# Performance work log

Hardware: AMD Instinct MI355X
Metric: run time of the kernel (lower is better)

The kernel has to match this reference:

```python
import jax, jax.numpy as jnp
import numpy as np

NUM_Q = 8
B, N, D = 8, 1024, 512
C = 1024


def setup_inputs() -> dict:
    key = jax.random.key(0)
    k1, k2 = jax.random.split(key)
    x = jax.random.normal(k1, (B, N, D), dtype=jnp.float32)
    codebooks = jax.random.normal(k2, (NUM_Q, C, D), dtype=jnp.float32)
    return {"x": x, "codebooks": codebooks}


def _vq_layer(residual, codebook):
    # residual: [b, n, d]; codebook: [c, d]
    # squared euclidean distances without materializing differences tensor
    r2 = jnp.sum(residual * residual, axis=-1, keepdims=True)          # [b, n, 1]
    e2 = jnp.sum(codebook * codebook, axis=-1)                          # [c]
    dots = jnp.einsum('bnd,cd->bnc', residual, codebook)                # [b, n, c]
    dist = r2 - 2.0 * dots + e2                                         # [b, n, c]
    indices = jnp.argmin(dist, axis=-1)                                 # [b, n] int32
    quantized = codebook[indices]                                       # [b, n, d]
    # straight-through estimator (codebook is EMA-updated, not differentiated)
    quantized_st = residual + jax.lax.stop_gradient(quantized - residual)
    # commitment loss (default commitment_weight = 1.0)
    loss = jnp.mean((jax.lax.stop_gradient(quantized_st) - residual) ** 2)
    return quantized_st, indices, loss


def reference(x, codebooks):
    def step(carry, codebook):
        residual, quantized_out = carry
        quantized, indices, loss = _vq_layer(residual, codebook)
        return (residual - quantized, quantized_out + quantized), (indices, loss)

    init = (x, jnp.zeros_like(x))
    (_, quantized_out), (all_indices, all_losses) = jax.lax.scan(step, init, codebooks)
    # all_indices: [q, b, n] -> [b, n, q]; all_losses: [q]
    all_indices = jnp.transpose(all_indices, (1, 2, 0))
    return quantized_out, all_indices, all_losses
```

## Files before the change

kernel.cpp:

```cpp
#include <hip/hip_runtime.h>
#include <float.h>

#define NUM_Q 8
#define BN    8192
#define D     512
#define C     1024

#define QOUT_OFF 0
#define IDX_OFF  (BN * D)
#define LOSS_OFF (IDX_OFF + BN * NUM_Q)

#define WIN_OFF_B  0
#define E2_OFF_B   (BN * 8)

typedef _Float16 f16x8 __attribute__((ext_vector_type(8)));
typedef float    f32x4 __attribute__((ext_vector_type(4)));

#define TM  128
#define TN  128
#define BKK 32
#define LDK 40
#define GTHREADS 512

__device__ __forceinline__ unsigned fkey(float f) {
    unsigned u = __float_as_uint(f);
    return (u & 0x80000000u) ? ~u : (u | 0x80000000u);
}

__device__ __forceinline__ unsigned long long u64min(unsigned long long a, unsigned long long b) {
    return a < b ? a : b;
}

__device__ __forceinline__ unsigned long long shfl_xor_u64(unsigned long long v, int m) {
    int lo = __shfl_xor((int)(unsigned)v, m, 64);
    int hi = __shfl_xor((int)(unsigned)(v >> 32), m, 64);
    return ((unsigned long long)(unsigned)hi << 32) | (unsigned)lo;
}

__global__ void rvq_init_kernel(const float* __restrict__ x, float* __restrict__ out,
                                unsigned long long* __restrict__ winners) {
    int i = blockIdx.x * blockDim.x + threadIdx.x;
    const float4* x4 = (const float4*)x;
    float4* r4 = (float4*)(out + QOUT_OFF);
    const int n4 = BN * D / 4;
    for (int k = i; k < n4; k += gridDim.x * blockDim.x)
        r4[k] = x4[k];
    if (i < BN) winners[i] = ~0ull;
    if (i < NUM_Q) out[LOSS_OFF + i] = 0.0f;
}

__global__ void rvq_e2_kernel(const float* __restrict__ cbs, float* __restrict__ e2ws) {
    const int row = blockIdx.x;
    const int lane = threadIdx.x;
    const float* p = cbs + (size_t)row * D + lane * 8;
    float4 a = *(const float4*)p;
    float4 b = *(const float4*)(p + 4);
    float ss = a.x*a.x + a.y*a.y + a.z*a.z + a.w*a.w
             + b.x*b.x + b.y*b.y + b.z*b.z + b.w*b.w;
#pragma unroll
    for (int off = 32; off >= 1; off >>= 1) ss += __shfl_xor(ss, off, 64);
    if (lane == 0) e2ws[row] = ss;
}

__global__ __launch_bounds__(GTHREADS, 4) void rvq_score_kernel(
    const float* __restrict__ cb,
    const float* __restrict__ R,
    const float* __restrict__ e2,
    unsigned long long* __restrict__ winners)
{
    __shared__ __align__(16) _Float16 AsHi[TM][LDK];
    __shared__ __align__(16) _Float16 AsLo[TM][LDK];
    __shared__ __align__(16) _Float16 BsHi[TN][LDK];
    __shared__ __align__(16) _Float16 BsLo[TN][LDK];
    __shared__ unsigned long long part[4][TM];

    const int tid  = threadIdx.x;
    const int lane = tid & 63;
    const int wv   = tid >> 6;
    const int wm   = wv & 1;
    const int wn   = wv >> 1;
    const int lm   = lane & 15;
    const int lq   = lane >> 4;

    const int mg = blockIdx.x & 63;
    const int nb = blockIdx.x >> 6;
    const int tok0 = mg * TM;
    const int cb0  = nb * TN;

    const int srow = tid >> 2;
    const int skq  = tid & 3;

    const float* Ag = R  + (size_t)(tok0 + srow) * D + skq * 8;
    const float* Bg = cb + (size_t)(cb0  + srow) * D + skq * 8;

    f32x4 acc[4][2];
#pragma unroll
    for (int mt = 0; mt < 4; ++mt)
#pragma unroll
        for (int nt = 0; nt < 2; ++nt)
            acc[mt][nt] = (f32x4){0.f, 0.f, 0.f, 0.f};

    for (int kb = 0; kb < D / BKK; ++kb) {
        const int kc = kb * BKK;
        float4 a0 = *(const float4*)(Ag + kc);
        float4 a1 = *(const float4*)(Ag + kc + 4);
        float4 b0 = *(const float4*)(Bg + kc);
        float4 b1 = *(const float4*)(Bg + kc + 4);

        __syncthreads();

        {
            float av[8] = {a0.x, a0.y, a0.z, a0.w, a1.x, a1.y, a1.z, a1.w};
            f16x8 h, l;
#pragma unroll
            for (int i = 0; i < 8; ++i) {
                _Float16 hi = (_Float16)av[i];
                h[i] = hi;
                l[i] = (_Float16)(av[i] - (float)hi);
            }
            *(f16x8*)&AsHi[srow][skq * 8] = h;
            *(f16x8*)&AsLo[srow][skq * 8] = l;
        }
        {
            float bv[8] = {b0.x, b0.y, b0.z, b0.w, b1.x, b1.y, b1.z, b1.w};
            f16x8 h, l;
#pragma unroll
            for (int i = 0; i < 8; ++i) {
                _Float16 hi = (_Float16)bv[i];
                h[i] = hi;
                l[i] = (_Float16)(bv[i] - (float)hi);
            }
            *(f16x8*)&BsHi[srow][skq * 8] = h;
            *(f16x8*)&BsLo[srow][skq * 8] = l;
        }
        __syncthreads();

        f16x8 ah[4], al[4], bh[2], bl[2];
#pragma unroll
        for (int mt = 0; mt < 4; ++mt) {
            ah[mt] = *(const f16x8*)&AsHi[wm * 64 + mt * 16 + lm][lq * 8];
            al[mt] = *(const f16x8*)&AsLo[wm * 64 + mt * 16 + lm][lq * 8];
        }
#pragma unroll
        for (int nt = 0; nt < 2; ++nt) {
            bh[nt] = *(const f16x8*)&BsHi[wn * 32 + nt * 16 + lm][lq * 8];
            bl[nt] = *(const f16x8*)&BsLo[wn * 32 + nt * 16 + lm][lq * 8];
        }
#pragma unroll
        for (int mt = 0; mt < 4; ++mt)
#pragma unroll
            for (int nt = 0; nt < 2; ++nt)
                acc[mt][nt] = __builtin_amdgcn_mfma_f32_16x16x32_f16(ah[mt], bh[nt], acc[mt][nt], 0, 0, 0);
#pragma unroll
        for (int mt = 0; mt < 4; ++mt)
#pragma unroll
            for (int nt = 0; nt < 2; ++nt)
                acc[mt][nt] = __builtin_amdgcn_mfma_f32_16x16x32_f16(ah[mt], bl[nt], acc[mt][nt], 0, 0, 0);
#pragma unroll
        for (int mt = 0; mt < 4; ++mt)
#pragma unroll
            for (int nt = 0; nt < 2; ++nt)
                acc[mt][nt] = __builtin_amdgcn_mfma_f32_16x16x32_f16(al[mt], bh[nt], acc[mt][nt], 0, 0, 0);
    }

    const int n0 = cb0 + wn * 32 + lm;
    const float e2v0 = e2[n0];
    const float e2v1 = e2[n0 + 16];

#pragma unroll
    for (int mt = 0; mt < 4; ++mt) {
#pragma unroll
        for (int r = 0; r < 4; ++r) {
            float s0 = e2v0 - 2.0f * acc[mt][0][r];
            float s1 = e2v1 - 2.0f * acc[mt][1][r];
            unsigned long long p0 = ((unsigned long long)fkey(s0) << 32) | (unsigned)n0;
            unsigned long long p1 = ((unsigned long long)fkey(s1) << 32) | (unsigned)(n0 + 16);
            unsigned long long p = u64min(p0, p1);
#pragma unroll
            for (int off = 1; off < 16; off <<= 1)
                p = u64min(p, shfl_xor_u64(p, off));
            if (lm == 0)
                part[wn][wm * 64 + mt * 16 + lq * 4 + r] = p;
        }
    }
    __syncthreads();
    if (tid < TM) {
        unsigned long long p = part[0][tid];
        p = u64min(p, part[1][tid]);
        p = u64min(p, part[2][tid]);
        p = u64min(p, part[3][tid]);
        atomicMin(&winners[tok0 + tid], p);
    }
}

__global__ __launch_bounds__(256) void rvq_update_kernel(
    const float* __restrict__ cb, float* __restrict__ out,
    unsigned long long* __restrict__ winners, int q)
{
    __shared__ float lsum[4];
    const int tid = threadIdx.x;
    const int tl  = tid >> 4;
    const int g   = tid & 15;
    const int tok = blockIdx.x * 16 + tl;

    float* R = out + QOUT_OFF;
    unsigned long long w = winners[tok];
    const int best = (int)(unsigned)(w & 0xFFFFFFFFull);
    const float* crow = cb + (size_t)best * D;
    float* rrow = R + (size_t)tok * D;

    float ss = 0.0f;
#pragma unroll
    for (int m = 0; m < 8; ++m) {
        const int off = (m * 16 + g) * 4;
        float4 r = *(const float4*)&rrow[off];
        float4 c = *(const float4*)&crow[off];
        float4 nr = make_float4(r.x - c.x, r.y - c.y, r.z - c.z, r.w - c.w);
        *(float4*)&rrow[off] = nr;
        ss += nr.x * nr.x + nr.y * nr.y + nr.z * nr.z + nr.w * nr.w;
    }
    if (g == 0) {
        out[IDX_OFF + (size_t)tok * NUM_Q + q] = (float)best;
        winners[tok] = ~0ull;
    }
#pragma unroll
    for (int off = 32; off >= 1; off >>= 1) ss += __shfl_xor(ss, off, 64);
    if ((tid & 63) == 0) lsum[tid >> 6] = ss;
    __syncthreads();
    if (tid == 0)
        atomicAdd(out + LOSS_OFF + q, lsum[0] + lsum[1] + lsum[2] + lsum[3]);
}

__global__ void rvq_finalize_kernel(const float* __restrict__ x, float* __restrict__ out) {
    int i = blockIdx.x * blockDim.x + threadIdx.x;
    const float4* x4 = (const float4*)x;
    float4* o4 = (float4*)(out + QOUT_OFF);
    const int n4 = BN * D / 4;
    for (int k = i; k < n4; k += gridDim.x * blockDim.x) {
        float4 xv = x4[k];
        float4 rv = o4[k];
        o4[k] = make_float4(xv.x - rv.x, xv.y - rv.y, xv.z - rv.z, xv.w - rv.w);
    }
    if (i < NUM_Q) out[LOSS_OFF + i] *= (1.0f / (float)(BN * D));
}

extern "C" void kernel_launch(void* const* d_in, const int* in_sizes, int n_in,
                              void* d_out, int out_size, void* d_ws, size_t ws_size,
                              hipStream_t stream) {
    const float* x   = (const float*)d_in[0];
    const float* cbs = (const float*)d_in[1];
    float* out = (float*)d_out;
    unsigned long long* winners = (unsigned long long*)((char*)d_ws + WIN_OFF_B);
    float* e2ws = (float*)((char*)d_ws + E2_OFF_B);

    hipLaunchKernelGGL(rvq_init_kernel, dim3(1024), dim3(256), 0, stream, x, out, winners);
    hipLaunchKernelGGL(rvq_e2_kernel, dim3(NUM_Q * C), dim3(64), 0, stream, cbs, e2ws);

    float* R = out + QOUT_OFF;
    for (int q = 0; q < NUM_Q; ++q) {
        const float* cb_q = cbs + (size_t)q * C * D;
        hipLaunchKernelGGL(rvq_score_kernel, dim3((BN / TM) * (C / TN)), dim3(GTHREADS), 0, stream,
                           cb_q, R, e2ws + (size_t)q * C, winners);
        hipLaunchKernelGGL(rvq_update_kernel, dim3(BN / 16), dim3(256), 0, stream,
                           cb_q, out, winners, q);
    }
    hipLaunchKernelGGL(rvq_finalize_kernel, dim3(1024), dim3(256), 0, stream, x, out);
}
```

Measured before the change: 455.1 us.

## Replace split-fp16 GEMM with fp16 top-2 shortlist and exact fp32 rescoring

The distance GEMM now uses a single fp16 pass instead of three hi/lo split MFMA passes, with a larger K tile. Each 128-code tile keeps its top-2 candidates per token, giving 16 candidates per token. A new fused kernel rescores those candidates exactly in fp32, then updates the residual and the loss. This cuts MFMA work and removes the atomicMin, but the argmin is only exact if the true winner lands in some tile's top-2 under fp16 error.

```diff
diff --git a/kernel.cpp b/kernel.cpp
--- a/kernel.cpp
+++ b/kernel.cpp
@@ -10,42 +10,41 @@
 #define IDX_OFF  (BN * D)
 #define LOSS_OFF (IDX_OFF + BN * NUM_Q)
 
-#define WIN_OFF_B  0
-#define E2_OFF_B   (BN * 8)
+#define TOP2_OFF_B 0
+#define E2_OFF_B   (BN * 16 * 8)
 
 typedef _Float16 f16x8 __attribute__((ext_vector_type(8)));
 typedef float    f32x4 __attribute__((ext_vector_type(4)));
 
-#define TM  128
-#define TN  128
-#define BKK 32
-#define LDK 40
+#define TM   128
+#define TN   128
+#define BK   64
+#define LDKA 72
 #define GTHREADS 512
 
 __device__ __forceinline__ unsigned fkey(float f) {
     unsigned u = __float_as_uint(f);
     return (u & 0x80000000u) ? ~u : (u | 0x80000000u);
 }
-
 __device__ __forceinline__ unsigned long long u64min(unsigned long long a, unsigned long long b) {
     return a < b ? a : b;
 }
-
+__device__ __forceinline__ unsigned long long u64max(unsigned long long a, unsigned long long b) {
+    return a > b ? a : b;
+}
 __device__ __forceinline__ unsigned long long shfl_xor_u64(unsigned long long v, int m) {
     int lo = __shfl_xor((int)(unsigned)v, m, 64);
     int hi = __shfl_xor((int)(unsigned)(v >> 32), m, 64);
     return ((unsigned long long)(unsigned)hi << 32) | (unsigned)lo;
 }
 
-__global__ void rvq_init_kernel(const float* __restrict__ x, float* __restrict__ out,
-                                unsigned long long* __restrict__ winners) {
+__global__ void rvq_init_kernel(const float* __restrict__ x, float* __restrict__ out) {
     int i = blockIdx.x * blockDim.x + threadIdx.x;
     const float4* x4 = (const float4*)x;
     float4* r4 = (float4*)(out + QOUT_OFF);
     const int n4 = BN * D / 4;
     for (int k = i; k < n4; k += gridDim.x * blockDim.x)
         r4[k] = x4[k];
-    if (i < BN) winners[i] = ~0ull;
     if (i < NUM_Q) out[LOSS_OFF + i] = 0.0f;
 }
 
@@ -62,17 +61,15 @@
     if (lane == 0) e2ws[row] = ss;
 }
 
-__global__ __launch_bounds__(GTHREADS, 4) void rvq_score_kernel(
+__global__ __launch_bounds__(GTHREADS, 4) void rvq_approx_kernel(
     const float* __restrict__ cb,
     const float* __restrict__ R,
     const float* __restrict__ e2,
-    unsigned long long* __restrict__ winners)
+    unsigned long long* __restrict__ top2)
 {
-    __shared__ __align__(16) _Float16 AsHi[TM][LDK];
-    __shared__ __align__(16) _Float16 AsLo[TM][LDK];
-    __shared__ __align__(16) _Float16 BsHi[TN][LDK];
-    __shared__ __align__(16) _Float16 BsLo[TN][LDK];
-    __shared__ unsigned long long part[4][TM];
+    __shared__ __align__(16) _Float16 As[TM][LDKA];
+    __shared__ __align__(16) _Float16 Bs[TN][LDKA];
+    __shared__ unsigned long long part[4][TM][2];
 
     const int tid  = threadIdx.x;
     const int lane = tid & 63;
@@ -88,10 +85,10 @@
     const int cb0  = nb * TN;
 
     const int srow = tid >> 2;
-    const int skq  = tid & 3;
-
-    const float* Ag = R  + (size_t)(tok0 + srow) * D + skq * 8;
-    const float* Bg = cb + (size_t)(cb0  + srow) * D + skq * 8;
+    const int sc   = tid & 3;
+
+    const float* Ag = R  + (size_t)(tok0 + srow) * D + sc * 16;
+    const float* Bg = cb + (size_t)(cb0  + srow) * D + sc * 16;
 
     f32x4 acc[4][2];
 #pragma unroll
@@ -100,67 +97,54 @@
         for (int nt = 0; nt < 2; ++nt)
             acc[mt][nt] = (f32x4){0.f, 0.f, 0.f, 0.f};
 
-    for (int kb = 0; kb < D / BKK; ++kb) {
-        const int kc = kb * BKK;
+    for (int kb = 0; kb < D / BK; ++kb) {
+        const int kc = kb * BK;
         float4 a0 = *(const float4*)(Ag + kc);
         float4 a1 = *(const float4*)(Ag + kc + 4);
+        float4 a2 = *(const float4*)(Ag + kc + 8);
+        float4 a3 = *(const float4*)(Ag + kc + 12);
         float4 b0 = *(const float4*)(Bg + kc);
         float4 b1 = *(const float4*)(Bg + kc + 4);
+        float4 b2 = *(const float4*)(Bg + kc + 8);
+        float4 b3 = *(const float4*)(Bg + kc + 12);
 
         __syncthreads();
 
         {
-            float av[8] = {a0.x, a0.y, a0.z, a0.w, a1.x, a1.y, a1.z, a1.w};
-            f16x8 h, l;
-#pragma unroll
-            for (int i = 0; i < 8; ++i) {
-                _Float16 hi = (_Float16)av[i];
-                h[i] = hi;
-                l[i] = (_Float16)(av[i] - (float)hi);
-            }
-            *(f16x8*)&AsHi[srow][skq * 8] = h;
-            *(f16x8*)&AsLo[srow][skq * 8] = l;
+            float av[16] = {a0.x,a0.y,a0.z,a0.w, a1.x,a1.y,a1.z,a1.w,
+                            a2.x,a2.y,a2.z,a2.w, a3.x,a3.y,a3.z,a3.w};
+            f16x8 h0, h1;
+#pragma unroll
+            for (int i = 0; i < 8; ++i) { h0[i] = (_Float16)av[i]; h1[i] = (_Float16)av[8+i]; }
+            *(f16x8*)&As[srow][sc * 16]     = h0;
+            *(f16x8*)&As[srow][sc * 16 + 8] = h1;
         }
         {
-            float bv[8] = {b0.x, b0.y, b0.z, b0.w, b1.x, b1.y, b1.z, b1.w};
-            f16x8 h, l;
-#pragma unroll
-            for (int i = 0; i < 8; ++i) {
-                _Float16 hi = (_Float16)bv[i];
-                h[i] = hi;
-                l[i] = (_Float16)(bv[i] - (float)hi);
-            }
-            *(f16x8*)&BsHi[srow][skq * 8] = h;
-            *(f16x8*)&BsLo[srow][skq * 8] = l;
+            float bv[16] = {b0.x,b0.y,b0.z,b0.w, b1.x,b1.y,b1.z,b1.w,
+                            b2.x,b2.y,b2.z,b2.w, b3.x,b3.y,b3.z,b3.w};
+            f16x8 h0, h1;
+#pragma unroll
+            for (int i = 0; i < 8; ++i) { h0[i] = (_Float16)bv[i]; h1[i] = (_Float16)bv[8+i]; }
+            *(f16x8*)&Bs[srow][sc * 16]     = h0;
+            *(f16x8*)&Bs[srow][sc * 16 + 8] = h1;
         }
         __syncthreads();
 
-        f16x8 ah[4], al[4], bh[2], bl[2];
-#pragma unroll
-        for (int mt = 0; mt < 4; ++mt) {
-            ah[mt] = *(const f16x8*)&AsHi[wm * 64 + mt * 16 + lm][lq * 8];
-            al[mt] = *(const f16x8*)&AsLo[wm * 64 + mt * 16 + lm][lq * 8];
-        }
-#pragma unroll
-        for (int nt = 0; nt < 2; ++nt) {
-            bh[nt] = *(const f16x8*)&BsHi[wn * 32 + nt * 16 + lm][lq * 8];
-            bl[nt] = *(const f16x8*)&BsLo[wn * 32 + nt * 16 + lm][lq * 8];
-        }
-#pragma unroll
-        for (int mt = 0; mt < 4; ++mt)
+#pragma unroll
+        for (int kh = 0; kh < 2; ++kh) {
+            f16x8 ah[4], bh[2];
+#pragma unroll
+            for (int mt = 0; mt < 4; ++mt)
+                ah[mt] = *(const f16x8*)&As[wm * 64 + mt * 16 + lm][kh * 32 + lq * 8];
 #pragma unroll
             for (int nt = 0; nt < 2; ++nt)
-                acc[mt][nt] = __builtin_amdgcn_mfma_f32_16x16x32_f16(ah[mt], bh[nt], acc[mt][nt], 0, 0, 0);
-#pragma unroll
-        for (int mt = 0; mt < 4; ++mt)
-#pragma unroll
-            for (int nt = 0; nt < 2; ++nt)
-                acc[mt][nt] = __builtin_amdgcn_mfma_f32_16x16x32_f16(ah[mt], bl[nt], acc[mt][nt], 0, 0, 0);
-#pragma unroll
-        for (int mt = 0; mt < 4; ++mt)
-#pragma unroll
-            for (int nt = 0; nt < 2; ++nt)
-                acc[mt][nt] = __builtin_amdgcn_mfma_f32_16x16x32_f16(al[mt], bh[nt], acc[mt][nt], 0, 0, 0);
+                bh[nt] = *(const f16x8*)&Bs[wn * 32 + nt * 16 + lm][kh * 32 + lq * 8];
+#pragma unroll
+            for (int mt = 0; mt < 4; ++mt)
+#pragma unroll
+                for (int nt = 0; nt < 2; ++nt)
+                    acc[mt][nt] = __builtin_amdgcn_mfma_f32_16x16x32_f16(ah[mt], bh[nt], acc[mt][nt], 0, 0, 0);
+        }
     }
 
     const int n0 = cb0 + wn * 32 + lm;
@@ -173,62 +157,100 @@
         for (int r = 0; r < 4; ++r) {
             float s0 = e2v0 - 2.0f * acc[mt][0][r];
             float s1 = e2v1 - 2.0f * acc[mt][1][r];
-            unsigned long long p0 = ((unsigned long long)fkey(s0) << 32) | (unsigned)n0;
-            unsigned long long p1 = ((unsigned long long)fkey(s1) << 32) | (unsigned)(n0 + 16);
-            unsigned long long p = u64min(p0, p1);
-#pragma unroll
-            for (int off = 1; off < 16; off <<= 1)
-                p = u64min(p, shfl_xor_u64(p, off));
-            if (lm == 0)
-                part[wn][wm * 64 + mt * 16 + lq * 4 + r] = p;
+            unsigned long long pa = ((unsigned long long)fkey(s0) << 32) | (unsigned)n0;
+            unsigned long long pb = ((unsigned long long)fkey(s1) << 32) | (unsigned)(n0 + 16);
+            unsigned long long lo = u64min(pa, pb);
+            unsigned long long hi = u64max(pa, pb);
+#pragma unroll
+            for (int m = 1; m < 16; m <<= 1) {
+                unsigned long long o1 = shfl_xor_u64(lo, m);
+                unsigned long long o2 = shfl_xor_u64(hi, m);
+                unsigned long long n1 = u64min(lo, o1);
+                unsigned long long n2 = u64min(u64max(lo, o1), u64min(hi, o2));
+                lo = n1; hi = n2;
+            }
+            if (lm == 0) {
+                const int trow = wm * 64 + mt * 16 + lq * 4 + r;
+                part[wn][trow][0] = lo;
+                part[wn][trow][1] = hi;
+            }
         }
     }
     __syncthreads();
     if (tid < TM) {
-        unsigned long long p = part[0][tid];
-        p = u64min(p, part[1][tid]);
-        p = u64min(p, part[2][tid]);
-        p = u64min(p, part[3][tid]);
-        atomicMin(&winners[tok0 + tid], p);
-    }
-}
-
-__global__ __launch_bounds__(256) void rvq_update_kernel(
-    const float* __restrict__ cb, float* __restrict__ out,
-    unsigned long long* __restrict__ winners, int q)
+        unsigned long long lo = part[0][tid][0];
+        unsigned long long hi = part[0][tid][1];
+#pragma unroll
+        for (int w = 1; w < 4; ++w) {
+            unsigned long long q1 = part[w][tid][0];
+            unsigned long long q2 = part[w][tid][1];
+            unsigned long long n1 = u64min(lo, q1);
+            unsigned long long n2 = u64min(u64max(lo, q1), u64min(hi, q2));
+            lo = n1; hi = n2;
+        }
+        unsigned long long* dst = top2 + (size_t)(tok0 + tid) * 16 + nb * 2;
+        dst[0] = lo;
+        dst[1] = hi;
+    }
+}
+
+__global__ __launch_bounds__(512) void rvq_rescore_update_kernel(
+    const float* __restrict__ cb, const float* __restrict__ e2,
+    const unsigned long long* __restrict__ top2,
+    float* __restrict__ out, int q)
 {
-    __shared__ float lsum[4];
-    const int tid = threadIdx.x;
-    const int tl  = tid >> 4;
-    const int g   = tid & 15;
-    const int tok = blockIdx.x * 16 + tl;
-
-    float* R = out + QOUT_OFF;
-    unsigned long long w = winners[tok];
-    const int best = (int)(unsigned)(w & 0xFFFFFFFFull);
-    const float* crow = cb + (size_t)best * D;
-    float* rrow = R + (size_t)tok * D;
-
-    float ss = 0.0f;
-#pragma unroll
-    for (int m = 0; m < 8; ++m) {
-        const int off = (m * 16 + g) * 4;
-        float4 r = *(const float4*)&rrow[off];
-        float4 c = *(const float4*)&crow[off];
-        float4 nr = make_float4(r.x - c.x, r.y - c.y, r.z - c.z, r.w - c.w);
-        *(float4*)&rrow[off] = nr;
-        ss += nr.x * nr.x + nr.y * nr.y + nr.z * nr.z + nr.w * nr.w;
-    }
-    if (g == 0) {
-        out[IDX_OFF + (size_t)tok * NUM_Q + q] = (float)best;
-        winners[tok] = ~0ull;
-    }
+    __shared__ float lsum[8];
+    const int tid  = threadIdx.x;
+    const int lane = tid & 63;
+    const int w    = tid >> 6;
+    const int tok  = blockIdx.x * 8 + w;
+
+    float* rrow = out + QOUT_OFF + (size_t)tok * D + lane * 8;
+    float4 r0 = *(const float4*)rrow;
+    float4 r1 = *(const float4*)(rrow + 4);
+
+    unsigned long long myc = top2[(size_t)tok * 16 + (lane & 15)];
+    int myidx = (int)(unsigned)(myc & 0xFFFFFFFFull);
+
+    unsigned long long best = ~0ull;
+#pragma unroll 4
+    for (int j = 0; j < 16; ++j) {
+        int idx = __shfl(myidx, j, 64);
+        const float* crow = cb + (size_t)idx * D + lane * 8;
+        float4 c0 = *(const float4*)crow;
+        float4 c1 = *(const float4*)(crow + 4);
+        float p = r0.x*c0.x + r0.y*c0.y + r0.z*c0.z + r0.w*c0.w
+                + r1.x*c1.x + r1.y*c1.y + r1.z*c1.z + r1.w*c1.w;
+#pragma unroll
+        for (int off = 32; off >= 1; off >>= 1) p += __shfl_xor(p, off, 64);
+        float s = e2[idx] - 2.0f * p;
+        unsigned long long key = ((unsigned long long)fkey(s) << 32) | (unsigned)idx;
+        best = u64min(best, key);
+    }
+
+    const int bi = (int)(unsigned)(best & 0xFFFFFFFFull);
+    const float* crow = cb + (size_t)bi * D + lane * 8;
+    float4 c0 = *(const float4*)crow;
+    float4 c1 = *(const float4*)(crow + 4);
+    float4 n0 = make_float4(r0.x - c0.x, r0.y - c0.y, r0.z - c0.z, r0.w - c0.w);
+    float4 n1 = make_float4(r1.x - c1.x, r1.y - c1.y, r1.z - c1.z, r1.w - c1.w);
+    *(float4*)rrow = n0;
+    *(float4*)(rrow + 4) = n1;
+    float ss = n0.x*n0.x + n0.y*n0.y + n0.z*n0.z + n0.w*n0.w
+             + n1.x*n1.x + n1.y*n1.y + n1.z*n1.z + n1.w*n1.w;
 #pragma unroll
     for (int off = 32; off >= 1; off >>= 1) ss += __shfl_xor(ss, off, 64);
-    if ((tid & 63) == 0) lsum[tid >> 6] = ss;
+    if (lane == 0) {
+        out[IDX_OFF + (size_t)tok * NUM_Q + q] = (float)bi;
+        lsum[w] = ss;
+    }
     __syncthreads();
-    if (tid == 0)
-        atomicAdd(out + LOSS_OFF + q, lsum[0] + lsum[1] + lsum[2] + lsum[3]);
+    if (tid == 0) {
+        float tot = 0.0f;
+#pragma unroll
+        for (int i = 0; i < 8; ++i) tot += lsum[i];
+        atomicAdd(out + LOSS_OFF + q, tot);
+    }
 }
 
 __global__ void rvq_finalize_kernel(const float* __restrict__ x, float* __restrict__ out) {
@@ -250,19 +272,19 @@
     const float* x   = (const float*)d_in[0];
     const float* cbs = (const float*)d_in[1];
     float* out = (float*)d_out;
-    unsigned long long* winners = (unsigned long long*)((char*)d_ws + WIN_OFF_B);
+    unsigned long long* top2 = (unsigned long long*)((char*)d_ws + TOP2_OFF_B);
     float* e2ws = (float*)((char*)d_ws + E2_OFF_B);
 
-    hipLaunchKernelGGL(rvq_init_kernel, dim3(1024), dim3(256), 0, stream, x, out, winners);
+    hipLaunchKernelGGL(rvq_init_kernel, dim3(1024), dim3(256), 0, stream, x, out);
     hipLaunchKernelGGL(rvq_e2_kernel, dim3(NUM_Q * C), dim3(64), 0, stream, cbs, e2ws);
 
     float* R = out + QOUT_OFF;
     for (int q = 0; q < NUM_Q; ++q) {
         const float* cb_q = cbs + (size_t)q * C * D;
-        hipLaunchKernelGGL(rvq_score_kernel, dim3((BN / TM) * (C / TN)), dim3(GTHREADS), 0, stream,
-                           cb_q, R, e2ws + (size_t)q * C, winners);
-        hipLaunchKernelGGL(rvq_update_kernel, dim3(BN / 16), dim3(256), 0, stream,
-                           cb_q, out, winners, q);
+        hipLaunchKernelGGL(rvq_approx_kernel, dim3((BN / TM) * (C / TN)), dim3(GTHREADS), 0, stream,
+                           cb_q, R, e2ws + (size_t)q * C, top2);
+        hipLaunchKernelGGL(rvq_rescore_update_kernel, dim3(BN / 8), dim3(512), 0, stream,
+                           cb_q, e2ws + (size_t)q * C, top2, out, q);
     }
     hipLaunchKernelGGL(rvq_finalize_kernel, dim3(1024), dim3(256), 0, stream, x, out);
 }
```

After: 562.6 us. +23.6%, slower.

## Fuse scoring, argmin and residual update into one per-layer kernel

Applied to the files above, without the earlier changes.

Replaces the separate score and update kernels with one kernel per layer. Each block holds 32 tokens' residual (hi/lo fp16 split) in LDS and sweeps the whole 1024-entry codebook, so the argmin finishes inside the block with no global atomicMin and no winners buffer. Codebooks are pre-split into fp16 hi/lo once in a prep kernel and streamed with global_load_lds into a swizzled LDS tile. The init copy is removed by reading x directly for the first layer. The cost is a grid of only 256 blocks and a larger LDS footprint per block, which may lower occupancy.

```diff
diff --git a/kernel.cpp b/kernel.cpp
--- a/kernel.cpp
+++ b/kernel.cpp
@@ -10,225 +10,234 @@
 #define IDX_OFF  (BN * D)
 #define LOSS_OFF (IDX_OFF + BN * NUM_Q)
 
-#define WIN_OFF_B  0
-#define E2_OFF_B   (BN * 8)
+#define CBHI_B 0
+#define CBLO_B (NUM_Q * C * D * 2)
+#define E2_B   (2 * NUM_Q * C * D * 2)
 
 typedef _Float16 f16x8 __attribute__((ext_vector_type(8)));
 typedef float    f32x4 __attribute__((ext_vector_type(4)));
 
-#define TM  128
-#define TN  128
-#define BKK 32
-#define LDK 40
-#define GTHREADS 512
+#define TPB     32
+#define THREADS 512
+#define GRID    (BN / TPB)
+#define BK      32
+#define NCHUNK  (D / BK)
+#define ALD     520
 
 __device__ __forceinline__ unsigned fkey(float f) {
     unsigned u = __float_as_uint(f);
     return (u & 0x80000000u) ? ~u : (u | 0x80000000u);
 }
-
 __device__ __forceinline__ unsigned long long u64min(unsigned long long a, unsigned long long b) {
     return a < b ? a : b;
 }
-
 __device__ __forceinline__ unsigned long long shfl_xor_u64(unsigned long long v, int m) {
     int lo = __shfl_xor((int)(unsigned)v, m, 64);
     int hi = __shfl_xor((int)(unsigned)(v >> 32), m, 64);
     return ((unsigned long long)(unsigned)hi << 32) | (unsigned)lo;
 }
-
-__global__ void rvq_init_kernel(const float* __restrict__ x, float* __restrict__ out,
-                                unsigned long long* __restrict__ winners) {
-    int i = blockIdx.x * blockDim.x + threadIdx.x;
-    const float4* x4 = (const float4*)x;
-    float4* r4 = (float4*)(out + QOUT_OFF);
-    const int n4 = BN * D / 4;
-    for (int k = i; k < n4; k += gridDim.x * blockDim.x)
-        r4[k] = x4[k];
-    if (i < BN) winners[i] = ~0ull;
-    if (i < NUM_Q) out[LOSS_OFF + i] = 0.0f;
-}
-
-__global__ void rvq_e2_kernel(const float* __restrict__ cbs, float* __restrict__ e2ws) {
+__device__ __forceinline__ void glds16(const void* g, void* l) {
+    __builtin_amdgcn_global_load_lds((const __attribute__((address_space(1))) void*)g,
+                                     (__attribute__((address_space(3))) void*)l, 16, 0, 0);
+}
+
+__global__ void rvq_prep_kernel(const float* __restrict__ cbs, char* __restrict__ ws,
+                                float* __restrict__ out) {
     const int row = blockIdx.x;
     const int lane = threadIdx.x;
+    _Float16* cbhi = (_Float16*)(ws + CBHI_B);
+    _Float16* cblo = (_Float16*)(ws + CBLO_B);
+    float* e2ws = (float*)(ws + E2_B);
+
     const float* p = cbs + (size_t)row * D + lane * 8;
     float4 a = *(const float4*)p;
     float4 b = *(const float4*)(p + 4);
-    float ss = a.x*a.x + a.y*a.y + a.z*a.z + a.w*a.w
-             + b.x*b.x + b.y*b.y + b.z*b.z + b.w*b.w;
+    float v[8] = {a.x, a.y, a.z, a.w, b.x, b.y, b.z, b.w};
+    f16x8 h, l;
+    float ss = 0.0f;
+#pragma unroll
+    for (int i = 0; i < 8; ++i) {
+        _Float16 hi = (_Float16)v[i];
+        h[i] = hi;
+        l[i] = (_Float16)(v[i] - (float)hi);
+        ss += v[i] * v[i];
+    }
+    *(f16x8*)(cbhi + (size_t)row * D + lane * 8) = h;
+    *(f16x8*)(cblo + (size_t)row * D + lane * 8) = l;
 #pragma unroll
     for (int off = 32; off >= 1; off >>= 1) ss += __shfl_xor(ss, off, 64);
     if (lane == 0) e2ws[row] = ss;
-}
-
-__global__ __launch_bounds__(GTHREADS, 4) void rvq_score_kernel(
-    const float* __restrict__ cb,
-    const float* __restrict__ R,
+    if (row == 0 && lane < NUM_Q) out[LOSS_OFF + lane] = 0.0f;
+}
+
+__global__ __launch_bounds__(THREADS, 2) void rvq_layer_kernel(
+    const float* __restrict__ Rsrc,
+    const _Float16* __restrict__ cbhi,
+    const _Float16* __restrict__ cblo,
+    const float* __restrict__ cbf,
     const float* __restrict__ e2,
-    unsigned long long* __restrict__ winners)
+    float* __restrict__ out, int q)
 {
-    __shared__ __align__(16) _Float16 AsHi[TM][LDK];
-    __shared__ __align__(16) _Float16 AsLo[TM][LDK];
-    __shared__ __align__(16) _Float16 BsHi[TN][LDK];
-    __shared__ __align__(16) _Float16 BsLo[TN][LDK];
-    __shared__ unsigned long long part[4][TM];
+    __shared__ __align__(16) _Float16 Ahi[TPB][ALD];
+    __shared__ __align__(16) _Float16 Alo[TPB][ALD];
+    __shared__ __align__(16) _Float16 Bsh[C * BK];
+    __shared__ unsigned long long part[8][TPB];
+    __shared__ int   bestIdx[TPB];
+    __shared__ float lsum[8];
 
     const int tid  = threadIdx.x;
     const int lane = tid & 63;
     const int wv   = tid >> 6;
-    const int wm   = wv & 1;
-    const int wn   = wv >> 1;
     const int lm   = lane & 15;
     const int lq   = lane >> 4;
-
-    const int mg = blockIdx.x & 63;
-    const int nb = blockIdx.x >> 6;
-    const int tok0 = mg * TM;
-    const int cb0  = nb * TN;
-
-    const int srow = tid >> 2;
-    const int skq  = tid & 3;
-
-    const float* Ag = R  + (size_t)(tok0 + srow) * D + skq * 8;
-    const float* Bg = cb + (size_t)(cb0  + srow) * D + skq * 8;
-
-    f32x4 acc[4][2];
-#pragma unroll
-    for (int mt = 0; mt < 4; ++mt)
-#pragma unroll
-        for (int nt = 0; nt < 2; ++nt)
-            acc[mt][nt] = (f32x4){0.f, 0.f, 0.f, 0.f};
-
-    for (int kb = 0; kb < D / BKK; ++kb) {
-        const int kc = kb * BKK;
-        float4 a0 = *(const float4*)(Ag + kc);
-        float4 a1 = *(const float4*)(Ag + kc + 4);
-        float4 b0 = *(const float4*)(Bg + kc);
-        float4 b1 = *(const float4*)(Bg + kc + 4);
-
-        __syncthreads();
-
-        {
-            float av[8] = {a0.x, a0.y, a0.z, a0.w, a1.x, a1.y, a1.z, a1.w};
+    const int tok0 = blockIdx.x * TPB;
+
+    {
+        const int t = tid >> 4;
+        const int g = tid & 15;
+        const float* rp = Rsrc + (size_t)(tok0 + t) * D + g * 32;
+#pragma unroll
+        for (int j = 0; j < 4; ++j) {
+            float4 v0 = *(const float4*)(rp + j * 8);
+            float4 v1 = *(const float4*)(rp + j * 8 + 4);
+            float v[8] = {v0.x, v0.y, v0.z, v0.w, v1.x, v1.y, v1.z, v1.w};
             f16x8 h, l;
 #pragma unroll
             for (int i = 0; i < 8; ++i) {
-                _Float16 hi = (_Float16)av[i];
+                _Float16 hi = (_Float16)v[i];
                 h[i] = hi;
-                l[i] = (_Float16)(av[i] - (float)hi);
+                l[i] = (_Float16)(v[i] - (float)hi);
             }
-            *(f16x8*)&AsHi[srow][skq * 8] = h;
-            *(f16x8*)&AsLo[srow][skq * 8] = l;
-        }
-        {
-            float bv[8] = {b0.x, b0.y, b0.z, b0.w, b1.x, b1.y, b1.z, b1.w};
-            f16x8 h, l;
-#pragma unroll
-            for (int i = 0; i < 8; ++i) {
-                _Float16 hi = (_Float16)bv[i];
-                h[i] = hi;
-                l[i] = (_Float16)(bv[i] - (float)hi);
+            *(f16x8*)&Ahi[t][g * 32 + j * 8] = h;
+            *(f16x8*)&Alo[t][g * 32 + j * 8] = l;
+        }
+    }
+
+    int grow[8], goct[8];
+#pragma unroll
+    for (int j = 0; j < 8; ++j) {
+        const int s = (wv * 8 + j) * 64 + lane;
+        grow[j] = s >> 2;
+        goct[j] = (s & 3) ^ ((s >> 2) & 3);
+    }
+
+    f32x4 acc[2][8];
+#pragma unroll
+    for (int mf = 0; mf < 2; ++mf)
+#pragma unroll
+        for (int nf = 0; nf < 8; ++nf)
+            acc[mf][nf] = (f32x4){0.f, 0.f, 0.f, 0.f};
+
+    for (int kb = 0; kb < NCHUNK; ++kb) {
+        const int kc = kb * BK;
+        f16x8 ah[2], al[2], bb[8];
+
+        __syncthreads();
+#pragma unroll
+        for (int j = 0; j < 8; ++j)
+            glds16(cbhi + (size_t)grow[j] * D + kc + goct[j] * 8,
+                   (char*)Bsh + ((wv * 8 + j) * 64 + lane) * 16);
+        __syncthreads();
+
+#pragma unroll
+        for (int mf = 0; mf < 2; ++mf) {
+            ah[mf] = *(const f16x8*)&Ahi[mf * 16 + lm][kc + lq * 8];
+            al[mf] = *(const f16x8*)&Alo[mf * 16 + lm][kc + lq * 8];
+        }
+#pragma unroll
+        for (int nf = 0; nf < 8; ++nf) {
+            const int col = wv * 128 + nf * 16 + lm;
+            bb[nf] = *(const f16x8*)((char*)Bsh + col * 64 + ((lq ^ (col & 3)) << 4));
+        }
+#pragma unroll
+        for (int mf = 0; mf < 2; ++mf)
+#pragma unroll
+            for (int nf = 0; nf < 8; ++nf) {
+                acc[mf][nf] = __builtin_amdgcn_mfma_f32_16x16x32_f16(ah[mf], bb[nf], acc[mf][nf], 0, 0, 0);
+                acc[mf][nf] = __builtin_amdgcn_mfma_f32_16x16x32_f16(al[mf], bb[nf], acc[mf][nf], 0, 0, 0);
             }
-            *(f16x8*)&BsHi[srow][skq * 8] = h;
-            *(f16x8*)&BsLo[srow][skq * 8] = l;
-        }
-        __syncthreads();
-
-        f16x8 ah[4], al[4], bh[2], bl[2];
-#pragma unroll
-        for (int mt = 0; mt < 4; ++mt) {
-            ah[mt] = *(const f16x8*)&AsHi[wm * 64 + mt * 16 + lm][lq * 8];
-            al[mt] = *(const f16x8*)&AsLo[wm * 64 + mt * 16 + lm][lq * 8];
-        }
-#pragma unroll
-        for (int nt = 0; nt < 2; ++nt) {
-            bh[nt] = *(const f16x8*)&BsHi[wn * 32 + nt * 16 + lm][lq * 8];
-            bl[nt] = *(const f16x8*)&BsLo[wn * 32 + nt * 16 + lm][lq * 8];
-        }
-#pragma unroll
-        for (int mt = 0; mt < 4; ++mt)
-#pragma unroll
-            for (int nt = 0; nt < 2; ++nt)
-                acc[mt][nt] = __builtin_amdgcn_mfma_f32_16x16x32_f16(ah[mt], bh[nt], acc[mt][nt], 0, 0, 0);
-#pragma unroll
-        for (int mt = 0; mt < 4; ++mt)
-#pragma unroll
-            for (int nt = 0; nt < 2; ++nt)
-                acc[mt][nt] = __builtin_amdgcn_mfma_f32_16x16x32_f16(ah[mt], bl[nt], acc[mt][nt], 0, 0, 0);
-#pragma unroll
-        for (int mt = 0; mt < 4; ++mt)
-#pragma unroll
-            for (int nt = 0; nt < 2; ++nt)
-                acc[mt][nt] = __builtin_amdgcn_mfma_f32_16x16x32_f16(al[mt], bh[nt], acc[mt][nt], 0, 0, 0);
-    }
-
-    const int n0 = cb0 + wn * 32 + lm;
-    const float e2v0 = e2[n0];
-    const float e2v1 = e2[n0 + 16];
-
-#pragma unroll
-    for (int mt = 0; mt < 4; ++mt) {
+
+        __syncthreads();
+#pragma unroll
+        for (int j = 0; j < 8; ++j)
+            glds16(cblo + (size_t)grow[j] * D + kc + goct[j] * 8,
+                   (char*)Bsh + ((wv * 8 + j) * 64 + lane) * 16);
+        __syncthreads();
+
+#pragma unroll
+        for (int nf = 0; nf < 8; ++nf) {
+            const int col = wv * 128 + nf * 16 + lm;
+            bb[nf] = *(const f16x8*)((char*)Bsh + col * 64 + ((lq ^ (col & 3)) << 4));
+        }
+#pragma unroll
+        for (int mf = 0; mf < 2; ++mf)
+#pragma unroll
+            for (int nf = 0; nf < 8; ++nf)
+                acc[mf][nf] = __builtin_amdgcn_mfma_f32_16x16x32_f16(ah[mf], bb[nf], acc[mf][nf], 0, 0, 0);
+    }
+
+    float e2v[8];
+#pragma unroll
+    for (int nf = 0; nf < 8; ++nf)
+        e2v[nf] = e2[wv * 128 + nf * 16 + lm];
+
+#pragma unroll
+    for (int mf = 0; mf < 2; ++mf) {
 #pragma unroll
         for (int r = 0; r < 4; ++r) {
-            float s0 = e2v0 - 2.0f * acc[mt][0][r];
-            float s1 = e2v1 - 2.0f * acc[mt][1][r];
-            unsigned long long p0 = ((unsigned long long)fkey(s0) << 32) | (unsigned)n0;
-            unsigned long long p1 = ((unsigned long long)fkey(s1) << 32) | (unsigned)(n0 + 16);
-            unsigned long long p = u64min(p0, p1);
-#pragma unroll
-            for (int off = 1; off < 16; off <<= 1)
-                p = u64min(p, shfl_xor_u64(p, off));
+            unsigned long long best = ~0ull;
+#pragma unroll
+            for (int nf = 0; nf < 8; ++nf) {
+                const int col = wv * 128 + nf * 16 + lm;
+                float s = e2v[nf] - 2.0f * acc[mf][nf][r];
+                best = u64min(best, ((unsigned long long)fkey(s) << 32) | (unsigned)col);
+            }
+#pragma unroll
+            for (int m = 1; m < 16; m <<= 1)
+                best = u64min(best, shfl_xor_u64(best, m));
             if (lm == 0)
-                part[wn][wm * 64 + mt * 16 + lq * 4 + r] = p;
+                part[wv][mf * 16 + lq * 4 + r] = best;
         }
     }
     __syncthreads();
-    if (tid < TM) {
-        unsigned long long p = part[0][tid];
-        p = u64min(p, part[1][tid]);
-        p = u64min(p, part[2][tid]);
-        p = u64min(p, part[3][tid]);
-        atomicMin(&winners[tok0 + tid], p);
-    }
-}
-
-__global__ __launch_bounds__(256) void rvq_update_kernel(
-    const float* __restrict__ cb, float* __restrict__ out,
-    unsigned long long* __restrict__ winners, int q)
-{
-    __shared__ float lsum[4];
-    const int tid = threadIdx.x;
-    const int tl  = tid >> 4;
-    const int g   = tid & 15;
-    const int tok = blockIdx.x * 16 + tl;
-
-    float* R = out + QOUT_OFF;
-    unsigned long long w = winners[tok];
-    const int best = (int)(unsigned)(w & 0xFFFFFFFFull);
-    const float* crow = cb + (size_t)best * D;
-    float* rrow = R + (size_t)tok * D;
-
-    float ss = 0.0f;
-#pragma unroll
-    for (int m = 0; m < 8; ++m) {
-        const int off = (m * 16 + g) * 4;
-        float4 r = *(const float4*)&rrow[off];
-        float4 c = *(const float4*)&crow[off];
-        float4 nr = make_float4(r.x - c.x, r.y - c.y, r.z - c.z, r.w - c.w);
-        *(float4*)&rrow[off] = nr;
-        ss += nr.x * nr.x + nr.y * nr.y + nr.z * nr.z + nr.w * nr.w;
-    }
-    if (g == 0) {
-        out[IDX_OFF + (size_t)tok * NUM_Q + q] = (float)best;
-        winners[tok] = ~0ull;
-    }
-#pragma unroll
-    for (int off = 32; off >= 1; off >>= 1) ss += __shfl_xor(ss, off, 64);
-    if ((tid & 63) == 0) lsum[tid >> 6] = ss;
+    if (tid < TPB) {
+        unsigned long long b = part[0][tid];
+#pragma unroll
+        for (int w = 1; w < 8; ++w) b = u64min(b, part[w][tid]);
+        bestIdx[tid] = (int)(unsigned)(b & 0xFFFFFFFFull);
+    }
     __syncthreads();
-    if (tid == 0)
-        atomicAdd(out + LOSS_OFF + q, lsum[0] + lsum[1] + lsum[2] + lsum[3]);
+
+    {
+        const int t = tid >> 4;
+        const int g = tid & 15;
+        const int tok = tok0 + t;
+        const int bi = bestIdx[t];
+        const float* crow = cbf + (size_t)bi * D + g * 32;
+        const float* rp   = Rsrc + (size_t)tok * D + g * 32;
+        float* wp         = out + QOUT_OFF + (size_t)tok * D + g * 32;
+        float ss = 0.0f;
+#pragma unroll
+        for (int j = 0; j < 8; ++j) {
+            float4 r = *(const float4*)(rp + j * 4);
+            float4 c = *(const float4*)(crow + j * 4);
+            float4 n = make_float4(r.x - c.x, r.y - c.y, r.z - c.z, r.w - c.w);
+            *(float4*)(wp + j * 4) = n;
+            ss += n.x * n.x + n.y * n.y + n.z * n.z + n.w * n.w;
+        }
+        if (g == 0)
+            out[IDX_OFF + (size_t)tok * NUM_Q + q] = (float)bi;
+#pragma unroll
+        for (int off = 32; off >= 1; off >>= 1) ss += __shfl_xor(ss, off, 64);
+        if (lane == 0) lsum[wv] = ss;
+    }
+    __syncthreads();
+    if (tid == 0) {
+        float tot = 0.0f;
+#pragma unroll
+        for (int i = 0; i < 8; ++i) tot += lsum[i];
+        atomicAdd(out + LOSS_OFF + q, tot);
+    }
 }
 
 __global__ void rvq_finalize_kernel(const float* __restrict__ x, float* __restrict__ out) {
@@ -250,19 +259,22 @@
     const float* x   = (const float*)d_in[0];
     const float* cbs = (const float*)d_in[1];
     float* out = (float*)d_out;
-    unsigned long long* winners = (unsigned long long*)((char*)d_ws + WIN_OFF_B);
-    float* e2ws = (float*)((char*)d_ws + E2_OFF_B);
-
-    hipLaunchKernelGGL(rvq_init_kernel, dim3(1024), dim3(256), 0, stream, x, out, winners);
-    hipLaunchKernelGGL(rvq_e2_kernel, dim3(NUM_Q * C), dim3(64), 0, stream, cbs, e2ws);
-
-    float* R = out + QOUT_OFF;
+    char* ws = (char*)d_ws;
+    _Float16* cbhi = (_Float16*)(ws + CBHI_B);
+    _Float16* cblo = (_Float16*)(ws + CBLO_B);
+    float* e2ws = (float*)(ws + E2_B);
+
+    hipLaunchKernelGGL(rvq_prep_kernel, dim3(NUM_Q * C), dim3(64), 0, stream, cbs, ws, out);
+
     for (int q = 0; q < NUM_Q; ++q) {
-        const float* cb_q = cbs + (size_t)q * C * D;
-        hipLaunchKernelGGL(rvq_score_kernel, dim3((BN / TM) * (C / TN)), dim3(GTHREADS), 0, stream,
-                           cb_q, R, e2ws + (size_t)q * C, winners);
-        hipLaunchKernelGGL(rvq_update_kernel, dim3(BN / 16), dim3(256), 0, stream,
-                           cb_q, out, winners, q);
+        const float* Rsrc = (q == 0) ? x : (out + QOUT_OFF);
+        hipLaunchKernelGGL(rvq_layer_kernel, dim3(GRID), dim3(THREADS), 0, stream,
+                           Rsrc,
+                           cbhi + (size_t)q * C * D,
+                           cblo + (size_t)q * C * D,
+                           cbs  + (size_t)q * C * D,
+                           e2ws + (size_t)q * C,
+                           out, q);
     }
     hipLaunchKernelGGL(rvq_finalize_kernel, dim3(1024), dim3(256), 0, stream, x, out);
 }
```

Result: slower. 674.9 us (+48.3%).
